# Kernel tuning notes

Hardware: AMD Instinct MI355X
Metric: run time of the kernel (lower is better)

Reference implementation:

```python
import jax, jax.numpy as jnp
import numpy as np

D = 256          # input_size
RNN = 256        # rnn_hidden
COND = 64        # cond_dim
HID = 128        # MLP hidden
N_FIXED = 128    # mask.sum() with alternating mask
N_FREE = D - N_FIXED
B = 131072

# Static index arrays implementing the boolean mask (even indices fixed).
IDX_FIXED = np.arange(0, D, 2)
IDX_FREE = np.arange(1, D, 2)


def setup_inputs() -> dict:
    key = jax.random.key(0)
    ks = jax.random.split(key, 8)
    in_dim = N_FIXED + RNN + COND  # 448
    x = jax.random.normal(ks[0], (B, D), jnp.float32)
    h = jax.random.normal(ks[1], (B, RNN + COND), jnp.float32)
    W1 = jax.random.normal(ks[2], (in_dim, HID), jnp.float32) / np.sqrt(in_dim)
    b1 = jnp.zeros((HID,), jnp.float32)
    W2 = jax.random.normal(ks[3], (HID, HID), jnp.float32) / np.sqrt(HID)
    b2 = jnp.zeros((HID,), jnp.float32)
    W3 = jax.random.normal(ks[4], (HID, N_FREE * 2), jnp.float32) / np.sqrt(HID)
    b3 = jnp.zeros((N_FREE * 2,), jnp.float32)
    return {"x": x, "h": h, "W1": W1, "b1": b1, "W2": W2, "b2": b2, "W3": W3, "b3": b3}


def reference(x, h, W1, b1, W2, b2, W3, b3):
    # gather fixed / free halves (static index gather == boolean-mask select)
    x_fixed = x[:, IDX_FIXED]          # [B, N_FIXED]
    x_free = x[:, IDX_FREE]            # [B, N_FREE]
    z = jnp.concatenate([x_fixed, h], axis=-1)  # [B, 448]
    a = jax.nn.relu(z @ W1 + b1)
    a = jax.nn.relu(a @ W2 + b2)
    st = a @ W3 + b3                   # [B, 2*N_FREE]
    s = jnp.tanh(st[:, :N_FREE])
    t = st[:, N_FREE:]
    y_free = x_free * jnp.exp(s) + t
    log_det = jnp.sum(s, axis=-1)
    # scatter-write back into output layout
    y = jnp.zeros_like(x).at[:, IDX_FIXED].set(x_fixed).at[:, IDX_FREE].set(y_free)
    return y, log_det
```

## Files before the change

kernel.cpp:

```cpp
#include <hip/hip_runtime.h>
#include <stdint.h>

typedef __attribute__((ext_vector_type(8))) short bf16x8;
typedef __attribute__((ext_vector_type(4))) float f32x4;

#define B_ROWS 131072
#define BM 64
#define ZP 456
#define AP 136

#define Z_OFF    0
#define Z_BYTES  (BM * ZP * 2)
#define A1_OFF   (Z_OFF + Z_BYTES)
#define A1_BYTES (BM * AP * 2)
#define BIAS_OFF (A1_OFF + A1_BYTES)
#define BIAS_BYTES (512 * 4)
#define LDET_OFF (BIAS_OFF + BIAS_BYTES)
#define LDS_TOTAL (LDET_OFF + 4 * 64 * 4)

#define W1P_OFF 0
#define W2P_OFF 7168
#define W3P_OFF 9216

__device__ inline uint16_t f2bf(float x) {
  uint32_t u = __float_as_uint(x);
  u += 0x7fffu + ((u >> 16) & 1u);
  return (uint16_t)(u >> 16);
}

__device__ inline float tanh_fast(float x) {
  x = fminf(fmaxf(x, -15.f), 15.f);
  float e = __expf(2.f * x);
  return (e - 1.f) / (e + 1.f);
}

__global__ void prepack_kernel(const float* __restrict__ W1,
                               const float* __restrict__ W2,
                               const float* __restrict__ W3,
                               uint4* __restrict__ wp) {
  int tid = blockIdx.x * 256 + threadIdx.x;
  if (tid >= 13312) return;
  int l = tid & 63, f = tid >> 6;
  const float* W; int N, kt, nt;
  if (f < 112)      { W = W1; N = 128; int ff = f;       nt = ff / 14; kt = ff - nt * 14; }
  else if (f < 144) { W = W2; N = 128; int ff = f - 112; nt = ff >> 2; kt = ff & 3; }
  else              { W = W3; N = 256; int ff = f - 144; nt = ff >> 2; kt = ff & 3; }
  int k0  = kt * 32 + (l >> 4) * 8;
  int col = nt * 16 + (l & 15);
  uint16_t v[8];
#pragma unroll
  for (int j = 0; j < 8; j++) v[j] = f2bf(W[(size_t)(k0 + j) * N + col]);
  uint4 o;
  o.x = (uint32_t)v[0] | ((uint32_t)v[1] << 16);
  o.y = (uint32_t)v[2] | ((uint32_t)v[3] << 16);
  o.z = (uint32_t)v[4] | ((uint32_t)v[5] << 16);
  o.w = (uint32_t)v[6] | ((uint32_t)v[7] << 16);
  wp[tid] = o;
}

__global__ __launch_bounds__(256, 2) void fused_kernel(
    const float* __restrict__ x, const float* __restrict__ h,
    const float* __restrict__ b1, const float* __restrict__ b2,
    const float* __restrict__ b3, const uint4* __restrict__ wp,
    float* __restrict__ y, float* __restrict__ ldet) {
  extern __shared__ uint8_t smem[];
  uint16_t* zs  = (uint16_t*)(smem + Z_OFF);
  uint16_t* a1  = (uint16_t*)(smem + A1_OFF);
  uint16_t* a2  = (uint16_t*)(smem + Z_OFF);
  float*    bias = (float*)(smem + BIAS_OFF);
  float*    lsum = (float*)(smem + LDET_OFF);

  const int t  = threadIdx.x;
  const int m0 = blockIdx.x * BM;

  for (int i = t; i < 512; i += 256)
    bias[i] = (i < 128) ? b1[i] : (i < 256) ? b2[i - 128] : b3[i - 256];

  {
    const float4* xg = (const float4*)(x + (size_t)m0 * 256);
#pragma unroll
    for (int k = 0; k < 16; k++) {
      int idx = t + k * 256;
      int row = idx >> 6, c4 = idx & 63;
      float4 v = xg[idx];
      uint32_t p = (uint32_t)f2bf(v.x) | ((uint32_t)f2bf(v.z) << 16);
      *(uint32_t*)&zs[row * ZP + c4 * 2] = p;
    }
    const float4* hg = (const float4*)(h + (size_t)m0 * 320);
#pragma unroll
    for (int k = 0; k < 20; k++) {
      int idx = t + k * 256;
      int row = idx / 80, c4 = idx - row * 80;
      float4 v = hg[idx];
      uint2 p;
      p.x = (uint32_t)f2bf(v.x) | ((uint32_t)f2bf(v.y) << 16);
      p.y = (uint32_t)f2bf(v.z) | ((uint32_t)f2bf(v.w) << 16);
      *(uint2*)&zs[row * ZP + 128 + c4 * 4] = p;
    }
  }
  __syncthreads();

  const int wid = t >> 6, l = t & 63;
  const int lr = l & 15, lq = l >> 4;

  {
    f32x4 acc[4][2] = {};
#pragma unroll 2
    for (int kt = 0; kt < 14; kt++) {
      bf16x8 afr[4];
#pragma unroll
      for (int mi = 0; mi < 4; mi++)
        afr[mi] = *(const bf16x8*)&zs[(mi * 16 + lr) * ZP + kt * 32 + lq * 8];
      bf16x8 bfr[2];
#pragma unroll
      for (int nj = 0; nj < 2; nj++)
        bfr[nj] = *(const bf16x8*)&wp[W1P_OFF + ((wid * 2 + nj) * 14 + kt) * 64 + l];
#pragma unroll
      for (int mi = 0; mi < 4; mi++)
#pragma unroll
        for (int nj = 0; nj < 2; nj++)
          acc[mi][nj] = __builtin_amdgcn_mfma_f32_16x16x32_bf16(afr[mi], bfr[nj], acc[mi][nj], 0, 0, 0);
    }
#pragma unroll
    for (int mi = 0; mi < 4; mi++)
#pragma unroll
      for (int nj = 0; nj < 2; nj++) {
        int col = wid * 32 + nj * 16 + lr;
        float bv = bias[col];
#pragma unroll
        for (int r = 0; r < 4; r++) {
          int row = mi * 16 + lq * 4 + r;
          a1[row * AP + col] = f2bf(fmaxf(acc[mi][nj][r] + bv, 0.f));
        }
      }
  }
  __syncthreads();

  {
    f32x4 acc[4][2] = {};
#pragma unroll
    for (int kt = 0; kt < 4; kt++) {
      bf16x8 afr[4];
#pragma unroll
      for (int mi = 0; mi < 4; mi++)
        afr[mi] = *(const bf16x8*)&a1[(mi * 16 + lr) * AP + kt * 32 + lq * 8];
      bf16x8 bfr[2];
#pragma unroll
      for (int nj = 0; nj < 2; nj++)
        bfr[nj] = *(const bf16x8*)&wp[W2P_OFF + ((wid * 2 + nj) * 4 + kt) * 64 + l];
#pragma unroll
      for (int mi = 0; mi < 4; mi++)
#pragma unroll
        for (int nj = 0; nj < 2; nj++)
          acc[mi][nj] = __builtin_amdgcn_mfma_f32_16x16x32_bf16(afr[mi], bfr[nj], acc[mi][nj], 0, 0, 0);
    }
    __syncthreads();
#pragma unroll
    for (int mi = 0; mi < 4; mi++)
#pragma unroll
      for (int nj = 0; nj < 2; nj++) {
        int col = wid * 32 + nj * 16 + lr;
        float bv = bias[128 + col];
#pragma unroll
        for (int r = 0; r < 4; r++) {
          int row = mi * 16 + lq * 4 + r;
          a2[row * AP + col] = f2bf(fmaxf(acc[mi][nj][r] + bv, 0.f));
        }
      }
  }
  __syncthreads();

  f32x4 acc3[4][4] = {};
#pragma unroll
  for (int kt = 0; kt < 4; kt++) {
    bf16x8 afr[4];
#pragma unroll
    for (int mi = 0; mi < 4; mi++)
      afr[mi] = *(const bf16x8*)&a2[(mi * 16 + lr) * AP + kt * 32 + lq * 8];
    bf16x8 bfr[4];
#pragma unroll
    for (int nj = 0; nj < 2; nj++) {
      bfr[nj]     = *(const bf16x8*)&wp[W3P_OFF + ((wid * 2 + nj) * 4 + kt) * 64 + l];
      bfr[nj + 2] = *(const bf16x8*)&wp[W3P_OFF + ((8 + wid * 2 + nj) * 4 + kt) * 64 + l];
    }
#pragma unroll
    for (int mi = 0; mi < 4; mi++)
#pragma unroll
      for (int nj = 0; nj < 4; nj++)
        acc3[mi][nj] = __builtin_amdgcn_mfma_f32_16x16x32_bf16(afr[mi], bfr[nj], acc3[mi][nj], 0, 0, 0);
  }

  float lp[4][4];
#pragma unroll
  for (int mi = 0; mi < 4; mi++)
#pragma unroll
    for (int r = 0; r < 4; r++) lp[mi][r] = 0.f;

#pragma unroll
  for (int mi = 0; mi < 4; mi++) {
#pragma unroll
    for (int nj = 0; nj < 2; nj++) {
      int colc = wid * 32 + nj * 16 + lr;
      float bs = bias[256 + colc];
      float bt = bias[384 + colc];
#pragma unroll
      for (int r = 0; r < 4; r++) {
        int grow = m0 + mi * 16 + lq * 4 + r;
        float sv = tanh_fast(acc3[mi][nj][r] + bs);
        float tv = acc3[mi][nj + 2][r] + bt;
        lp[mi][r] += sv;
        const float2 xv = *(const float2*)(x + (size_t)grow * 256 + 2 * colc);
        float2 o;
        o.x = xv.x;
        o.y = xv.y * __expf(sv) + tv;
        *(float2*)(y + (size_t)grow * 256 + 2 * colc) = o;
      }
    }
  }

#pragma unroll
  for (int mi = 0; mi < 4; mi++)
#pragma unroll
    for (int r = 0; r < 4; r++) {
      float v = lp[mi][r];
      v += __shfl_xor(v, 1);
      v += __shfl_xor(v, 2);
      v += __shfl_xor(v, 4);
      v += __shfl_xor(v, 8);
      if (lr == 0) lsum[wid * 64 + mi * 16 + lq * 4 + r] = v;
    }
  __syncthreads();
  if (t < 64) ldet[m0 + t] = lsum[t] + lsum[64 + t] + lsum[128 + t] + lsum[192 + t];
}

extern "C" void kernel_launch(void* const* d_in, const int* in_sizes, int n_in,
                              void* d_out, int out_size, void* d_ws, size_t ws_size,
                              hipStream_t stream) {
  const float* x  = (const float*)d_in[0];
  const float* h  = (const float*)d_in[1];
  const float* W1 = (const float*)d_in[2];
  const float* b1 = (const float*)d_in[3];
  const float* W2 = (const float*)d_in[4];
  const float* b2 = (const float*)d_in[5];
  const float* W3 = (const float*)d_in[6];
  const float* b3 = (const float*)d_in[7];
  float* y    = (float*)d_out;
  float* ldet = y + (size_t)B_ROWS * 256;
  uint4* wp   = (uint4*)d_ws;

  prepack_kernel<<<52, 256, 0, stream>>>(W1, W2, W3, wp);

  hipFuncSetAttribute((const void*)fused_kernel,
                      hipFuncAttributeMaxDynamicSharedMemorySize, LDS_TOTAL);
  fused_kernel<<<B_ROWS / BM, 256, LDS_TOTAL, stream>>>(x, h, b1, b2, b3, wp, y, ldet);
}
```

Measured before the change: 134.7 us.

## Shrink row tile to 16 and raise occupancy to 8 blocks per CU

New measurement: 181.0 us. 34.4% more time.

```diff
diff --git a/kernel.cpp b/kernel.cpp
--- a/kernel.cpp
+++ b/kernel.cpp
@@ -5,18 +5,15 @@
 typedef __attribute__((ext_vector_type(4))) float f32x4;
 
 #define B_ROWS 131072
-#define BM 64
+#define BM 16
 #define ZP 456
 #define AP 136
 
-#define Z_OFF    0
 #define Z_BYTES  (BM * ZP * 2)
-#define A1_OFF   (Z_OFF + Z_BYTES)
+#define A1_OFF   Z_BYTES
 #define A1_BYTES (BM * AP * 2)
-#define BIAS_OFF (A1_OFF + A1_BYTES)
-#define BIAS_BYTES (512 * 4)
-#define LDET_OFF (BIAS_OFF + BIAS_BYTES)
-#define LDS_TOTAL (LDET_OFF + 4 * 64 * 4)
+#define LDET_OFF (A1_OFF + A1_BYTES)
+#define LDS_TOTAL (LDET_OFF + 64 * 4)
 
 #define W1P_OFF 0
 #define W2P_OFF 7168
@@ -58,28 +55,24 @@
   wp[tid] = o;
 }
 
-__global__ __launch_bounds__(256, 2) void fused_kernel(
+__global__ __launch_bounds__(256, 8) void fused_kernel(
     const float* __restrict__ x, const float* __restrict__ h,
     const float* __restrict__ b1, const float* __restrict__ b2,
     const float* __restrict__ b3, const uint4* __restrict__ wp,
     float* __restrict__ y, float* __restrict__ ldet) {
   extern __shared__ uint8_t smem[];
-  uint16_t* zs  = (uint16_t*)(smem + Z_OFF);
-  uint16_t* a1  = (uint16_t*)(smem + A1_OFF);
-  uint16_t* a2  = (uint16_t*)(smem + Z_OFF);
-  float*    bias = (float*)(smem + BIAS_OFF);
+  uint16_t* zs   = (uint16_t*)smem;
+  uint16_t* a1   = (uint16_t*)(smem + A1_OFF);
+  uint16_t* a2   = zs;
   float*    lsum = (float*)(smem + LDET_OFF);
 
   const int t  = threadIdx.x;
   const int m0 = blockIdx.x * BM;
 
-  for (int i = t; i < 512; i += 256)
-    bias[i] = (i < 128) ? b1[i] : (i < 256) ? b2[i - 128] : b3[i - 256];
-
   {
     const float4* xg = (const float4*)(x + (size_t)m0 * 256);
 #pragma unroll
-    for (int k = 0; k < 16; k++) {
+    for (int k = 0; k < 4; k++) {
       int idx = t + k * 256;
       int row = idx >> 6, c4 = idx & 63;
       float4 v = xg[idx];
@@ -88,7 +81,7 @@
     }
     const float4* hg = (const float4*)(h + (size_t)m0 * 320);
 #pragma unroll
-    for (int k = 0; k < 20; k++) {
+    for (int k = 0; k < 5; k++) {
       int idx = t + k * 256;
       int row = idx / 80, c4 = idx - row * 80;
       float4 v = hg[idx];
@@ -104,133 +97,94 @@
   const int lr = l & 15, lq = l >> 4;
 
   {
-    f32x4 acc[4][2] = {};
+    f32x4 acc[2] = {};
 #pragma unroll 2
     for (int kt = 0; kt < 14; kt++) {
-      bf16x8 afr[4];
-#pragma unroll
-      for (int mi = 0; mi < 4; mi++)
-        afr[mi] = *(const bf16x8*)&zs[(mi * 16 + lr) * ZP + kt * 32 + lq * 8];
-      bf16x8 bfr[2];
-#pragma unroll
-      for (int nj = 0; nj < 2; nj++)
-        bfr[nj] = *(const bf16x8*)&wp[W1P_OFF + ((wid * 2 + nj) * 14 + kt) * 64 + l];
-#pragma unroll
-      for (int mi = 0; mi < 4; mi++)
-#pragma unroll
-        for (int nj = 0; nj < 2; nj++)
-          acc[mi][nj] = __builtin_amdgcn_mfma_f32_16x16x32_bf16(afr[mi], bfr[nj], acc[mi][nj], 0, 0, 0);
-    }
-#pragma unroll
-    for (int mi = 0; mi < 4; mi++)
-#pragma unroll
-      for (int nj = 0; nj < 2; nj++) {
-        int col = wid * 32 + nj * 16 + lr;
-        float bv = bias[col];
-#pragma unroll
-        for (int r = 0; r < 4; r++) {
-          int row = mi * 16 + lq * 4 + r;
-          a1[row * AP + col] = f2bf(fmaxf(acc[mi][nj][r] + bv, 0.f));
-        }
-      }
+      bf16x8 afr = *(const bf16x8*)&zs[lr * ZP + kt * 32 + lq * 8];
+      bf16x8 bfr0 = *(const bf16x8*)&wp[W1P_OFF + ((wid * 2 + 0) * 14 + kt) * 64 + l];
+      bf16x8 bfr1 = *(const bf16x8*)&wp[W1P_OFF + ((wid * 2 + 1) * 14 + kt) * 64 + l];
+      acc[0] = __builtin_amdgcn_mfma_f32_16x16x32_bf16(afr, bfr0, acc[0], 0, 0, 0);
+      acc[1] = __builtin_amdgcn_mfma_f32_16x16x32_bf16(afr, bfr1, acc[1], 0, 0, 0);
+    }
+#pragma unroll
+    for (int nj = 0; nj < 2; nj++) {
+      int col = wid * 32 + nj * 16 + lr;
+      float bv = b1[col];
+#pragma unroll
+      for (int r = 0; r < 4; r++)
+        a1[(lq * 4 + r) * AP + col] = f2bf(fmaxf(acc[nj][r] + bv, 0.f));
+    }
   }
   __syncthreads();
 
   {
-    f32x4 acc[4][2] = {};
+    f32x4 acc[2] = {};
 #pragma unroll
     for (int kt = 0; kt < 4; kt++) {
-      bf16x8 afr[4];
-#pragma unroll
-      for (int mi = 0; mi < 4; mi++)
-        afr[mi] = *(const bf16x8*)&a1[(mi * 16 + lr) * AP + kt * 32 + lq * 8];
-      bf16x8 bfr[2];
-#pragma unroll
-      for (int nj = 0; nj < 2; nj++)
-        bfr[nj] = *(const bf16x8*)&wp[W2P_OFF + ((wid * 2 + nj) * 4 + kt) * 64 + l];
-#pragma unroll
-      for (int mi = 0; mi < 4; mi++)
-#pragma unroll
-        for (int nj = 0; nj < 2; nj++)
-          acc[mi][nj] = __builtin_amdgcn_mfma_f32_16x16x32_bf16(afr[mi], bfr[nj], acc[mi][nj], 0, 0, 0);
+      bf16x8 afr = *(const bf16x8*)&a1[lr * AP + kt * 32 + lq * 8];
+      bf16x8 bfr0 = *(const bf16x8*)&wp[W2P_OFF + ((wid * 2 + 0) * 4 + kt) * 64 + l];
+      bf16x8 bfr1 = *(const bf16x8*)&wp[W2P_OFF + ((wid * 2 + 1) * 4 + kt) * 64 + l];
+      acc[0] = __builtin_amdgcn_mfma_f32_16x16x32_bf16(afr, bfr0, acc[0], 0, 0, 0);
+      acc[1] = __builtin_amdgcn_mfma_f32_16x16x32_bf16(afr, bfr1, acc[1], 0, 0, 0);
     }
     __syncthreads();
 #pragma unroll
-    for (int mi = 0; mi < 4; mi++)
-#pragma unroll
-      for (int nj = 0; nj < 2; nj++) {
-        int col = wid * 32 + nj * 16 + lr;
-        float bv = bias[128 + col];
-#pragma unroll
-        for (int r = 0; r < 4; r++) {
-          int row = mi * 16 + lq * 4 + r;
-          a2[row * AP + col] = f2bf(fmaxf(acc[mi][nj][r] + bv, 0.f));
-        }
-      }
-  }
-  __syncthreads();
-
-  f32x4 acc3[4][4] = {};
+    for (int nj = 0; nj < 2; nj++) {
+      int col = wid * 32 + nj * 16 + lr;
+      float bv = b2[col];
+#pragma unroll
+      for (int r = 0; r < 4; r++)
+        a2[(lq * 4 + r) * AP + col] = f2bf(fmaxf(acc[nj][r] + bv, 0.f));
+    }
+  }
+  __syncthreads();
+
+  f32x4 acc3[4] = {};
 #pragma unroll
   for (int kt = 0; kt < 4; kt++) {
-    bf16x8 afr[4];
-#pragma unroll
-    for (int mi = 0; mi < 4; mi++)
-      afr[mi] = *(const bf16x8*)&a2[(mi * 16 + lr) * AP + kt * 32 + lq * 8];
-    bf16x8 bfr[4];
-#pragma unroll
-    for (int nj = 0; nj < 2; nj++) {
-      bfr[nj]     = *(const bf16x8*)&wp[W3P_OFF + ((wid * 2 + nj) * 4 + kt) * 64 + l];
-      bfr[nj + 2] = *(const bf16x8*)&wp[W3P_OFF + ((8 + wid * 2 + nj) * 4 + kt) * 64 + l];
-    }
-#pragma unroll
-    for (int mi = 0; mi < 4; mi++)
-#pragma unroll
-      for (int nj = 0; nj < 4; nj++)
-        acc3[mi][nj] = __builtin_amdgcn_mfma_f32_16x16x32_bf16(afr[mi], bfr[nj], acc3[mi][nj], 0, 0, 0);
-  }
-
-  float lp[4][4];
-#pragma unroll
-  for (int mi = 0; mi < 4; mi++)
-#pragma unroll
-    for (int r = 0; r < 4; r++) lp[mi][r] = 0.f;
-
-#pragma unroll
-  for (int mi = 0; mi < 4; mi++) {
-#pragma unroll
-    for (int nj = 0; nj < 2; nj++) {
-      int colc = wid * 32 + nj * 16 + lr;
-      float bs = bias[256 + colc];
-      float bt = bias[384 + colc];
-#pragma unroll
-      for (int r = 0; r < 4; r++) {
-        int grow = m0 + mi * 16 + lq * 4 + r;
-        float sv = tanh_fast(acc3[mi][nj][r] + bs);
-        float tv = acc3[mi][nj + 2][r] + bt;
-        lp[mi][r] += sv;
-        const float2 xv = *(const float2*)(x + (size_t)grow * 256 + 2 * colc);
-        float2 o;
-        o.x = xv.x;
-        o.y = xv.y * __expf(sv) + tv;
-        *(float2*)(y + (size_t)grow * 256 + 2 * colc) = o;
-      }
-    }
-  }
-
-#pragma unroll
-  for (int mi = 0; mi < 4; mi++)
+    bf16x8 afr = *(const bf16x8*)&a2[lr * AP + kt * 32 + lq * 8];
+    bf16x8 bfrS0 = *(const bf16x8*)&wp[W3P_OFF + ((wid * 2 + 0) * 4 + kt) * 64 + l];
+    bf16x8 bfrS1 = *(const bf16x8*)&wp[W3P_OFF + ((wid * 2 + 1) * 4 + kt) * 64 + l];
+    bf16x8 bfrT0 = *(const bf16x8*)&wp[W3P_OFF + ((8 + wid * 2 + 0) * 4 + kt) * 64 + l];
+    bf16x8 bfrT1 = *(const bf16x8*)&wp[W3P_OFF + ((8 + wid * 2 + 1) * 4 + kt) * 64 + l];
+    acc3[0] = __builtin_amdgcn_mfma_f32_16x16x32_bf16(afr, bfrS0, acc3[0], 0, 0, 0);
+    acc3[1] = __builtin_amdgcn_mfma_f32_16x16x32_bf16(afr, bfrS1, acc3[1], 0, 0, 0);
+    acc3[2] = __builtin_amdgcn_mfma_f32_16x16x32_bf16(afr, bfrT0, acc3[2], 0, 0, 0);
+    acc3[3] = __builtin_amdgcn_mfma_f32_16x16x32_bf16(afr, bfrT1, acc3[3], 0, 0, 0);
+  }
+
+  float lp[4] = {0.f, 0.f, 0.f, 0.f};
+#pragma unroll
+  for (int nj = 0; nj < 2; nj++) {
+    int colc = wid * 32 + nj * 16 + lr;
+    float bs = b3[colc];
+    float bt = b3[128 + colc];
 #pragma unroll
     for (int r = 0; r < 4; r++) {
-      float v = lp[mi][r];
-      v += __shfl_xor(v, 1);
-      v += __shfl_xor(v, 2);
-      v += __shfl_xor(v, 4);
-      v += __shfl_xor(v, 8);
-      if (lr == 0) lsum[wid * 64 + mi * 16 + lq * 4 + r] = v;
-    }
-  __syncthreads();
-  if (t < 64) ldet[m0 + t] = lsum[t] + lsum[64 + t] + lsum[128 + t] + lsum[192 + t];
+      int grow = m0 + lq * 4 + r;
+      float sv = tanh_fast(acc3[nj][r] + bs);
+      float tv = acc3[nj + 2][r] + bt;
+      lp[r] += sv;
+      const float2 xv = *(const float2*)(x + (size_t)grow * 256 + 2 * colc);
+      float2 o;
+      o.x = xv.x;
+      o.y = xv.y * __expf(sv) + tv;
+      *(float2*)(y + (size_t)grow * 256 + 2 * colc) = o;
+    }
+  }
+
+#pragma unroll
+  for (int r = 0; r < 4; r++) {
+    float v = lp[r];
+    v += __shfl_xor(v, 1);
+    v += __shfl_xor(v, 2);
+    v += __shfl_xor(v, 4);
+    v += __shfl_xor(v, 8);
+    if (lr == 0) lsum[wid * BM + lq * 4 + r] = v;
+  }
+  __syncthreads();
+  if (t < BM)
+    ldet[m0 + t] = lsum[t] + lsum[BM + t] + lsum[2 * BM + t] + lsum[3 * BM + t];
 }
 
 extern "C" void kernel_launch(void* const* d_in, const int* in_sizes, int n_in,
@@ -250,7 +204,7 @@
 
   prepack_kernel<<<52, 256, 0, stream>>>(W1, W2, W3, wp);
 
-  hipFuncSetAttribute((const void*)fused_kernel,
-                      hipFuncAttributeMaxDynamicSharedMemorySize, LDS_TOTAL);
+  (void)hipFuncSetAttribute((const void*)fused_kernel,
+                            hipFuncAttributeMaxDynamicSharedMemorySize, LDS_TOTAL);
   fused_kernel<<<B_ROWS / BM, 256, LDS_TOTAL, stream>>>(x, h, b1, b2, b3, wp, y, ldet);
 }
```
